# Optimization experiments

Measured on AMD Instinct MI355X. Metric: run time of the kernel, lower is better.

## Reference

```python
import jax, jax.numpy as jnp
import numpy as np

D_MODEL = 1024
N_HEADS = 16
D_K = D_MODEL // N_HEADS
THETA = 10000.0
BATCH, SEQ = 2, 2048


def setup_inputs() -> dict:
    key = jax.random.key(0)
    k1, k2, k3 = jax.random.split(key, 3)
    std_qkv = float(np.sqrt(2.0 / (3 * D_MODEL + D_MODEL)))
    std_o = float(np.sqrt(2.0 / (D_MODEL + D_MODEL)))
    return {
        "x": jax.random.normal(k1, (BATCH, SEQ, D_MODEL), dtype=jnp.float32),
        "w_qkv": jax.random.normal(k2, (3 * D_MODEL, D_MODEL), dtype=jnp.float32) * std_qkv,
        "w_o": jax.random.normal(k3, (D_MODEL, D_MODEL), dtype=jnp.float32) * std_o,
        "token_positions": jnp.arange(SEQ, dtype=jnp.int32),
    }


def _rope(x, token_positions):
    # x: [..., s, d_k]; interleaved rotary embedding
    d_k = x.shape[-1]
    freqs = jnp.arange(0, d_k, 2, dtype=jnp.float32) / d_k          # [d_k/2]
    inv_freqs = 1.0 / (THETA ** freqs)
    angles = token_positions.astype(jnp.float32)[:, None] * inv_freqs  # [s, d_k/2]
    cos, sin = jnp.cos(angles), jnp.sin(angles)
    x_even, x_odd = x[..., 0::2], x[..., 1::2]
    rot_even = x_even * cos - x_odd * sin
    rot_odd = x_even * sin + x_odd * cos
    # interleave back: out[..., 2i] = rot_even[i], out[..., 2i+1] = rot_odd[i]
    return jnp.stack([rot_even, rot_odd], axis=-1).reshape(x.shape)


def reference(x, w_qkv, w_o, token_positions):
    b, s, _ = x.shape
    qkv = jnp.einsum('oi,bsi->bso', w_qkv, x)                        # [b, s, 3*d_model]
    q, k, v = jnp.split(qkv, 3, axis=-1)
    def to_heads(t):
        return t.reshape(b, s, N_HEADS, D_K).transpose(0, 2, 1, 3)  # [b, h, s, d]
    q, k, v = to_heads(q), to_heads(k), to_heads(v)
    q = _rope(q, token_positions)
    k = _rope(k, token_positions)
    scores = jnp.einsum('bhqd,bhkd->bhqk', q, k) / jnp.sqrt(jnp.float32(D_K))
    causal = jnp.tril(jnp.ones((s, s), dtype=bool))
    scores = jnp.where(causal, scores, -jnp.inf)
    attn = jax.nn.softmax(scores, axis=-1)
    y = jnp.einsum('bhqk,bhkd->bhqd', attn, v)
    y = y.transpose(0, 2, 1, 3).reshape(b, s, D_MODEL)
    return jnp.einsum('oi,bsi->bso', w_o, y)
```

## Files before the change

kernel.cpp:

```cpp
#include <hip/hip_runtime.h>
#include <math.h>

#define DEV __device__ __forceinline__

typedef __attribute__((ext_vector_type(8))) short bf16x8;
typedef __attribute__((ext_vector_type(4))) float f32x4;
typedef __attribute__((ext_vector_type(4))) unsigned int u32x4;

typedef __attribute__((address_space(3))) unsigned int lds_u32;
typedef const __attribute__((address_space(1))) unsigned int glb_u32;

DEV void gload16(const unsigned short* g, unsigned short* l) {
  __builtin_amdgcn_global_load_lds((glb_u32*)g, (lds_u32*)l, 16, 0, 0);
}

DEV bf16x8 lds_read8(const unsigned short* base, unsigned int byteoff) {
  return *reinterpret_cast<const bf16x8*>(
      reinterpret_cast<const char*>(base) + byteoff);
}

DEV float fexp2(float x) { return __builtin_amdgcn_exp2f(x); }

DEV unsigned short f2bf(float f) {
  union { float f; unsigned int u; } v; v.f = f;
  unsigned int u = v.u;
  unsigned int r = (u + 0x7fffu + ((u >> 16) & 1u)) >> 16;
  return (unsigned short)r;
}
DEV float bf2f(unsigned short h) {
  union { unsigned int u; float f; } v; v.u = ((unsigned int)h) << 16;
  return v.f;
}
DEV unsigned int cvtpk_bf16(float lo, float hi) {
  unsigned int r;
  asm("v_cvt_pk_bf16_f32 %0, %1, %2" : "=v"(r) : "v"(lo), "v"(hi));
  return r;
}

__global__ void cvt3_f32_bf16(const float* __restrict__ ina,
                              unsigned short* __restrict__ outa, int n4a,
                              const float* __restrict__ inb,
                              unsigned short* __restrict__ outb, int n4b,
                              const float* __restrict__ inc,
                              unsigned short* __restrict__ outc, int n4c) {
  int stride = gridDim.x * blockDim.x;
  int total = n4a + n4b + n4c;
  for (int i = blockIdx.x * blockDim.x + threadIdx.x; i < total; i += stride) {
    const float* src;
    unsigned short* dst;
    int j = i;
    if (j < n4a) {
      src = ina; dst = outa;
    } else if ((j -= n4a) < n4b) {
      src = inb; dst = outb;
    } else {
      j -= n4b; src = inc; dst = outc;
    }
    float4 f = reinterpret_cast<const float4*>(src)[j];
    ushort4 o;
    o.x = f2bf(f.x); o.y = f2bf(f.y); o.z = f2bf(f.z); o.w = f2bf(f.w);
    reinterpret_cast<ushort4*>(dst)[j] = o;
  }
}

__global__ __launch_bounds__(512, 2) void gemm8_qkv(const unsigned short* __restrict__ A,
                                                    const unsigned short* __restrict__ B,
                                                    unsigned short* __restrict__ C) {
  constexpr int K = 1024;
  constexpr int NK = 16;
  __shared__ unsigned short Ls[2][32768];

  const int tid = threadIdx.x;
  const int lane = tid & 63, wid = tid >> 6;
  const int wm = (wid >> 2) * 128;
  const int wn = (wid & 3) * 64;
  const int fr = lane & 15, kq = lane >> 4;

  int bid = blockIdx.x;
  int swz = (bid & 7) * 24 + (bid >> 3);
  int tm = swz & 15, tn = swz >> 4;
  const int arow0 = tm * 256, brow0 = tn * 256;

  const int subrow = lane >> 3;
  const int scol = ((lane & 7) ^ subrow) * 8;
  const unsigned short* aSrc = A + (size_t)(arow0 + wid * 8 + subrow) * K + scol;
  const unsigned short* bSrc = B + (size_t)(brow0 + wid * 8 + subrow) * K + scol;

  unsigned aoff[2], boff[2];
#pragma unroll
  for (int ks = 0; ks < 2; ks++) {
    unsigned x = ((unsigned)((ks * 4 + kq) ^ (fr & 7))) * 16;
    aoff[ks] = (unsigned)((wm + fr) * 128) + x;
    boff[ks] = 32768u + (unsigned)((wn + fr) * 128) + x;
  }

  f32x4 acc[8][4] = {};

#define STAGE_A8(BUF, H, T)                                                  \
  {                                                                          \
    gload16(aSrc + (size_t)((H) * 128) * K + (T) * 64,                       \
            &Ls[BUF][((H) * 128 + wid * 8) * 64]);                           \
    gload16(aSrc + (size_t)((H) * 128 + 64) * K + (T) * 64,                  \
            &Ls[BUF][((H) * 128 + 64 + wid * 8) * 64]);                      \
  }
#define STAGE_B8(BUF, H, T)                                                  \
  {                                                                          \
    gload16(bSrc + (size_t)((H) * 128) * K + (T) * 64,                       \
            &Ls[BUF][16384 + ((H) * 128 + wid * 8) * 64]);                   \
    gload16(bSrc + (size_t)((H) * 128 + 64) * K + (T) * 64,                  \
            &Ls[BUF][16384 + ((H) * 128 + 64 + wid * 8) * 64]);              \
  }

  STAGE_A8(0, 0, 0) STAGE_A8(0, 1, 0)
  STAGE_B8(0, 0, 0) STAGE_B8(0, 1, 0)
  STAGE_B8(1, 0, 1) STAGE_B8(1, 1, 1)
  asm volatile("s_waitcnt vmcnt(4)" ::: "memory");
  __builtin_amdgcn_s_barrier();

#define PHASE8(BUF, P, DO_STAGE)                                              \
  {                                                                           \
    bf16x8 af[2][2];                                                          \
    _Pragma("unroll") for (int mm = 0; mm < 2; mm++)                          \
      _Pragma("unroll") for (int ks = 0; ks < 2; ks++)                        \
        af[mm][ks] = lds_read8(Ls[BUF], aoff[ks] + ((P) * 2 + mm) * 2048);    \
    DO_STAGE                                                                  \
    __builtin_amdgcn_s_setprio(1);                                            \
    _Pragma("unroll") for (int mm = 0; mm < 2; mm++)                          \
      _Pragma("unroll") for (int j = 0; j < 4; j++)                           \
        _Pragma("unroll") for (int ks = 0; ks < 2; ks++)                      \
          acc[(P) * 2 + mm][j] = __builtin_amdgcn_mfma_f32_16x16x32_bf16(     \
              af[mm][ks], bq[j][ks], acc[(P) * 2 + mm][j], 0, 0, 0);          \
    __builtin_amdgcn_s_setprio(0);                                            \
  }

#define TILE8(T, BUF)                                                          \
  {                                                                            \
    bf16x8 bq[4][2];                                                           \
    _Pragma("unroll") for (int j = 0; j < 4; j++)                              \
      _Pragma("unroll") for (int ks = 0; ks < 2; ks++)                         \
        bq[j][ks] = lds_read8(Ls[BUF], boff[ks] + j * 2048);                   \
    PHASE8(BUF, 0, {                                                           \
      if ((T) + 1 < NK) { STAGE_A8(BUF ^ 1, 0, (T) + 1) STAGE_A8(BUF ^ 1, 1, (T) + 1) } \
    })                                                                         \
    __builtin_amdgcn_s_barrier();                                              \
    PHASE8(BUF, 1, { if ((T) + 2 < NK) STAGE_B8(BUF, 0, (T) + 2) })            \
    __builtin_amdgcn_s_barrier();                                              \
    PHASE8(BUF, 2, { if ((T) + 2 < NK) STAGE_B8(BUF, 1, (T) + 2) })            \
    __builtin_amdgcn_s_barrier();                                              \
    PHASE8(BUF, 3, {})                                                         \
    if ((T) + 2 < NK) {                                                        \
      asm volatile("s_waitcnt vmcnt(4)" ::: "memory");                         \
    } else {                                                                   \
      asm volatile("s_waitcnt vmcnt(0)" ::: "memory");                         \
    }                                                                          \
    __builtin_amdgcn_s_barrier();                                              \
    __builtin_amdgcn_sched_barrier(0);                                         \
  }

#pragma unroll 1
  for (int t = 0; t < NK; t += 2) {
    TILE8(t, 0)
    TILE8(t + 1, 1)
  }
#undef TILE8
#undef PHASE8
#undef STAGE_A8
#undef STAGE_B8

#pragma unroll
  for (int m = 0; m < 8; m++) {
#pragma unroll
    for (int j = 0; j < 4; j++) {
      size_t row = (size_t)(arow0 + wm + m * 16 + kq * 4);
      size_t col = (size_t)(brow0 + wn + j * 16 + fr);
#pragma unroll
      for (int r = 0; r < 4; r++)
        C[(row + r) * 3072 + col] = f2bf(acc[m][j][r]);
    }
  }
}

__global__ __launch_bounds__(256) void gemm_wo(const unsigned short* __restrict__ A,
                                               const unsigned short* __restrict__ B,
                                               float* __restrict__ C, int K) {
  __shared__ unsigned short Ab[2][4096];
  __shared__ unsigned short Bb[2][2048];
  const int tid = threadIdx.x;
  const int lane = tid & 63, wid = tid >> 6;
  const int wm = (wid >> 1) * 64, wn = (wid & 1) * 32;
  const int fr = lane & 15, kq = lane >> 4;
  const int arow0 = blockIdx.x * 128;
  const int brow0 = blockIdx.y * 64;

  const int srow = tid >> 2;
  const int schunk = (tid & 3) ^ (srow & 3);
  const unsigned short* aptr = A + (size_t)(arow0 + srow) * K + schunk * 8;
  const unsigned short* bptr = B + (size_t)(brow0 + srow) * K + schunk * 8;

  unsigned int offa[4], offb[2];
#pragma unroll
  for (int i = 0; i < 4; i++)
    offa[i] = (unsigned)((wm + i * 16 + fr) * 64 + ((kq ^ (fr & 3)) * 16));
#pragma unroll
  for (int j = 0; j < 2; j++)
    offb[j] = (unsigned)((wn + j * 16 + fr) * 64 + ((kq ^ (fr & 3)) * 16));

  f32x4 acc[4][2] = {};

#define WSTAGE(BI)                                                 \
  {                                                                \
    gload16(aptr, &Ab[BI][wid * 512]);                             \
    gload16(aptr + (size_t)64 * K, &Ab[BI][2048 + wid * 512]);     \
    gload16(bptr, &Bb[BI][wid * 512]);                             \
    aptr += 32;                                                    \
    bptr += 32;                                                    \
  }

#define WCOMP(BI)                                                                      \
  {                                                                                    \
    bf16x8 af[4], bfr[2];                                                              \
    _Pragma("unroll") for (int i = 0; i < 4; i++) af[i] = lds_read8(Ab[BI], offa[i]);  \
    _Pragma("unroll") for (int j = 0; j < 2; j++) bfr[j] = lds_read8(Bb[BI], offb[j]); \
    _Pragma("unroll") for (int i = 0; i < 4; i++)                                      \
      _Pragma("unroll") for (int j = 0; j < 2; j++)                                    \
        acc[i][j] = __builtin_amdgcn_mfma_f32_16x16x32_bf16(af[i], bfr[j], acc[i][j], 0, 0, 0); \
  }

  const int nk = K >> 5;
  WSTAGE(0);
  for (int ks = 0; ks < nk; ks += 2) {
    asm volatile("s_waitcnt lgkmcnt(0)" ::: "memory");
    __builtin_amdgcn_s_barrier();
    WSTAGE(1);
    asm volatile("s_waitcnt vmcnt(3)" ::: "memory");
    WCOMP(0);
    asm volatile("s_waitcnt lgkmcnt(0)" ::: "memory");
    __builtin_amdgcn_s_barrier();
    if (ks + 2 < nk) {
      WSTAGE(0);
      asm volatile("s_waitcnt vmcnt(3)" ::: "memory");
    } else {
      asm volatile("s_waitcnt vmcnt(0)" ::: "memory");
    }
    WCOMP(1);
  }
#undef WSTAGE
#undef WCOMP

#pragma unroll
  for (int i = 0; i < 4; i++) {
#pragma unroll
    for (int j = 0; j < 2; j++) {
#pragma unroll
      for (int r = 0; r < 4; r++) {
        size_t row = (size_t)(arow0 + wm + i * 16 + kq * 4 + r);
        size_t col = (size_t)(brow0 + wn + j * 16 + fr);
        C[row * 1024 + col] = acc[i][j][r];
      }
    }
  }
}

__global__ __launch_bounds__(256) void rope_vtrans_kernel(unsigned short* __restrict__ qkv,
                                                          const int* __restrict__ pos,
                                                          unsigned short* __restrict__ vt) {
  int bid0 = blockIdx.x;
  int t = threadIdx.x;
  if (bid0 < 4096) {
    int m = bid0;
    int s = m & 2047;
    __shared__ float Cl[32], Sl[32];
    if (t < 32) {
      float position = (float)pos[s];
      float inv = __expf(-(float)t * (9.210340371976184f / 32.0f));
      float ang = position * inv;
      Cl[t] = cosf(ang);
      Sl[t] = sinf(ang);
    }
    __syncthreads();
    const float QS = 0.18033688011112042f;
    int h = t >> 4, g = t & 15;
    float c0 = Cl[2 * g], s0 = Sl[2 * g], c1 = Cl[2 * g + 1], s1 = Sl[2 * g + 1];
    size_t base = (size_t)m * 3072 + h * 64 + 4 * g;
    ushort4 qv = *reinterpret_cast<ushort4*>(&qkv[base]);
    float qe0 = bf2f(qv.x), qo0 = bf2f(qv.y), qe1 = bf2f(qv.z), qo1 = bf2f(qv.w);
    qv.x = f2bf((qe0 * c0 - qo0 * s0) * QS);
    qv.y = f2bf((qe0 * s0 + qo0 * c0) * QS);
    qv.z = f2bf((qe1 * c1 - qo1 * s1) * QS);
    qv.w = f2bf((qe1 * s1 + qo1 * c1) * QS);
    *reinterpret_cast<ushort4*>(&qkv[base]) = qv;
    size_t kb = base + 1024;
    ushort4 kv = *reinterpret_cast<ushort4*>(&qkv[kb]);
    float ke0 = bf2f(kv.x), ko0 = bf2f(kv.y), ke1 = bf2f(kv.z), ko1 = bf2f(kv.w);
    kv.x = f2bf(ke0 * c0 - ko0 * s0);
    kv.y = f2bf(ke0 * s0 + ko0 * c0);
    kv.z = f2bf(ke1 * c1 - ko1 * s1);
    kv.w = f2bf(ke1 * s1 + ko1 * c1);
    *reinterpret_cast<ushort4*>(&qkv[kb]) = kv;
  } else {
    int bid = bid0 - 4096;
    int sb = bid & 31;
    int bh = bid >> 5;
    int h = bh & 15, b = bh >> 4;
    __shared__ unsigned short tile[64][72];
    int sl = t >> 2, c0 = (t & 3) * 16;
    const unsigned short* src = qkv + (size_t)(b * 2048 + sb * 64) * 3072 + 2048 + h * 64;
    *reinterpret_cast<bf16x8*>(&tile[sl][c0]) =
        *reinterpret_cast<const bf16x8*>(&src[(size_t)sl * 3072 + c0]);
    *reinterpret_cast<bf16x8*>(&tile[sl][c0 + 8]) =
        *reinterpret_cast<const bf16x8*>(&src[(size_t)sl * 3072 + c0 + 8]);
    __syncthreads();
    int d = t >> 2, p0 = (t & 3) * 16;
    unsigned short* dst = vt + ((size_t)bh * 64 + d) * 2048 + sb * 64 + p0;
    bf16x8 o0, o1;
#pragma unroll
    for (int i = 0; i < 8; i++) {
      int p = p0 + i;
      int s_in = (p & 32) + ((p >> 2) & 1) * 16 + ((p >> 3) & 3) * 4 + (p & 3);
      o0[i] = (short)tile[s_in][d];
    }
#pragma unroll
    for (int i = 0; i < 8; i++) {
      int p = p0 + 8 + i;
      int s_in = (p & 32) + ((p >> 2) & 1) * 16 + ((p >> 3) & 3) * 4 + (p & 3);
      o1[i] = (short)tile[s_in][d];
    }
    *reinterpret_cast<bf16x8*>(dst) = o0;
    *reinterpret_cast<bf16x8*>(dst + 8) = o1;
  }
}

__global__ __launch_bounds__(256, 4) void attn_kernel(const unsigned short* __restrict__ qkv,
                                                      const unsigned short* __restrict__ vt,
                                                      unsigned short* __restrict__ Y,
                                                      unsigned short* __restrict__ Opart,
                                                      float* __restrict__ Lsum) {
  int bid = blockIdx.x;
  int bh = bid & 31;
  int pair = (bid >> 5) & 15;
  int halfsel = bid >> 9;
  int h = bh & 15, b = bh >> 4;
  int tid = threadIdx.x, lane = tid & 63, wid = tid >> 6;
  int fr = lane & 15, kq = lane >> 4;

  const size_t mrow0 = (size_t)b * 2048;
  const unsigned short* Kp = qkv + mrow0 * 3072 + 1024 + h * 64;
  const unsigned short* Vp = vt + ((size_t)bh * 64) * 2048;

  __shared__ unsigned short Klds[2][4096];
  __shared__ unsigned short Vlds[2][4096];

  const int srow = tid >> 3;
  const int schunk = (tid & 7) ^ (srow & 7);

  unsigned int offk[8], offv[8];
#pragma unroll
  for (int gg = 0; gg < 4; gg++)
#pragma unroll
    for (int ks = 0; ks < 2; ks++) {
      int R = gg * 16 + fr;
      offk[gg * 2 + ks] = (unsigned)(R * 128 + (((4 * ks + kq) ^ (R & 7)) * 16));
    }
#pragma unroll
  for (int db = 0; db < 4; db++)
#pragma unroll
    for (int hf = 0; hf < 2; hf++) {
      int d = db * 16 + fr;
      offv[db * 2 + hf] = (unsigned)(d * 128 + (((4 * hf + kq) ^ (d & 7)) * 16));
    }

  bf16x8 vones;
#pragma unroll
  for (int i = 0; i < 8; i++) vones[i] = (short)0x3F80;

#define STAGE(BI)                                                     \
  {                                                                   \
    gload16(kstage, &Klds[BI][wid * 512]);                            \
    gload16(kstage + (size_t)32 * 3072, &Klds[BI][2048 + wid * 512]); \
    gload16(vstage, &Vlds[BI][wid * 512]);                            \
    gload16(vstage + 32 * 2048, &Vlds[BI][2048 + wid * 512]);         \
    kstage += (size_t)64 * 3072;                                      \
    vstage += 64;                                                     \
  }

#define TILE_COMPUTE(T, BI)                                                           \
  {                                                                                   \
    const bool masked_ = ((T) == qt_);                                                \
    f32x4 sc[4] = {};                                                                 \
    __builtin_amdgcn_s_setprio(1);                                                    \
    _Pragma("unroll") for (int gg = 0; gg < 4; gg++) {                                \
      _Pragma("unroll") for (int ks = 0; ks < 2; ks++) {                              \
        bf16x8 kf = lds_read8(Klds[BI], offk[gg * 2 + ks]);                           \
        sc[gg] = __builtin_amdgcn_mfma_f32_16x16x32_bf16(kf, qf[ks], sc[gg], 0, 0, 0);\
      }                                                                               \
    }                                                                                 \
    __builtin_amdgcn_s_setprio(0);                                                    \
    float p[16];                                                                      \
    _Pragma("unroll") for (int gg = 0; gg < 4; gg++)                                  \
      _Pragma("unroll") for (int rr = 0; rr < 4; rr++) {                              \
        float v = sc[gg][rr];                                                         \
        if (masked_) {                                                                \
          int k = (T) * 64 + gg * 16 + kq * 4 + rr;                                   \
          if (k > q_lane_) v = -1e30f;                                                \
        }                                                                             \
        p[gg * 4 + rr] = fexp2(v);                                                    \
      }                                                                               \
    u32x4 W0 = {cvtpk_bf16(p[0], p[1]), cvtpk_bf16(p[2], p[3]),                       \
                cvtpk_bf16(p[4], p[5]), cvtpk_bf16(p[6], p[7])};                      \
    u32x4 W1 = {cvtpk_bf16(p[8], p[9]), cvtpk_bf16(p[10], p[11]),                     \
                cvtpk_bf16(p[12], p[13]), cvtpk_bf16(p[14], p[15])};                  \
    bf16x8 pa0 = *reinterpret_cast<bf16x8*>(&W0);                                     \
    bf16x8 pa1 = *reinterpret_cast<bf16x8*>(&W1);                                     \
    __builtin_amdgcn_s_setprio(1);                                                    \
    _Pragma("unroll") for (int db = 0; db < 4; db++) {                                \
      bf16x8 vf0 = lds_read8(Vlds[BI], offv[db * 2]);                                 \
      acc[db] = __builtin_amdgcn_mfma_f32_16x16x32_bf16(vf0, pa0, acc[db], 0, 0, 0);  \
      bf16x8 vf1 = lds_read8(Vlds[BI], offv[db * 2 + 1]);                             \
      acc[db] = __builtin_amdgcn_mfma_f32_16x16x32_bf16(vf1, pa1, acc[db], 0, 0, 0);  \
    }                                                                                 \
    lacc = __builtin_amdgcn_mfma_f32_16x16x32_bf16(vones, pa0, lacc, 0, 0, 0);        \
    lacc = __builtin_amdgcn_mfma_f32_16x16x32_bf16(vones, pa1, lacc, 0, 0, 0);        \
    __builtin_amdgcn_s_setprio(0);                                                    \
  }

#define ATTN_RANGE(QT_, TLO_, THI_, MODE_, HALF_)                                     \
  {                                                                                   \
    const int qt_ = (QT_);                                                            \
    const int qbase_ = qt_ * 64 + wid * 16;                                           \
    const int q_lane_ = qbase_ + fr;                                                  \
    const unsigned short* Qp = qkv + (mrow0 + qbase_) * 3072 + h * 64;                \
    bf16x8 qf[2];                                                                     \
    _Pragma("unroll") for (int ks = 0; ks < 2; ks++)                                  \
      qf[ks] = *reinterpret_cast<const bf16x8*>(                                      \
          &Qp[(size_t)fr * 3072 + ks * 32 + kq * 8]);                                 \
    const unsigned short* kstage =                                                    \
        Kp + (size_t)srow * 3072 + schunk * 8 + (size_t)(TLO_) * 64 * 3072;           \
    const unsigned short* vstage =                                                    \
        Vp + (size_t)srow * 2048 + schunk * 8 + (TLO_) * 64;                          \
    f32x4 acc[4] = {};                                                                \
    f32x4 lacc = {};                                                                  \
    const int nt_ = (THI_) - (TLO_);                                                  \
    STAGE(0);                                                                         \
    for (int u = 0; u < nt_; u += 2) {                                                \
      asm volatile("s_waitcnt lgkmcnt(0)" ::: "memory");                              \
      __builtin_amdgcn_s_barrier();                                                   \
      if (u + 1 < nt_) {                                                              \
        STAGE(1);                                                                     \
        asm volatile("s_waitcnt vmcnt(4)" ::: "memory");                              \
      } else {                                                                        \
        asm volatile("s_waitcnt vmcnt(0)" ::: "memory");                              \
      }                                                                               \
      TILE_COMPUTE((TLO_) + u, 0);                                                    \
      if (u + 1 >= nt_) break;                                                        \
      asm volatile("s_waitcnt lgkmcnt(0)" ::: "memory");                              \
      __builtin_amdgcn_s_barrier();                                                   \
      if (u + 2 < nt_) {                                                              \
        STAGE(0);                                                                     \
        asm volatile("s_waitcnt vmcnt(4)" ::: "memory");                              \
      } else {                                                                        \
        asm volatile("s_waitcnt vmcnt(0)" ::: "memory");                              \
      }                                                                               \
      TILE_COMPUTE((TLO_) + u + 1, 1);                                                \
    }                                                                                 \
    if (MODE_ == 0) {                                                                 \
      float inv = 1.0f / lacc[0];                                                     \
      unsigned short* yp = Y + (mrow0 + qbase_ + fr) * 1024 + h * 64 + kq * 4;        \
      _Pragma("unroll") for (int db = 0; db < 4; db++) {                              \
        ushort4 o;                                                                    \
        o.x = f2bf(acc[db][0] * inv);                                                 \
        o.y = f2bf(acc[db][1] * inv);                                                 \
        o.z = f2bf(acc[db][2] * inv);                                                 \
        o.w = f2bf(acc[db][3] * inv);                                                 \
        *reinterpret_cast<ushort4*>(yp + db * 16) = o;                                \
      }                                                                               \
    } else {                                                                          \
      const int slot = (pair * 2 + (HALF_)) * 32 + bh;                                \
      unsigned short* op = Opart + (size_t)slot * 4096;                               \
      _Pragma("unroll") for (int db = 0; db < 4; db++)                                \
        _Pragma("unroll") for (int rr = 0; rr < 4; rr++) {                            \
          int d = db * 16 + kq * 4 + rr;                                              \
          op[(wid * 16 + 0) * 0 + d * 64 + (qbase_ & 63) + fr - (qbase_ & 63)] =      \
              f2bf(acc[db][rr]);                                                      \
        }                                                                             \
      if (kq == 0) Lsum[slot * 256 + wid * 16 + 0 * 64 + (fr) + wid * 0] = lacc[0];   \
    }                                                                                 \
  }


  if (halfsel == 0) {
    const int Lt = 31 - pair;
    {
      const int qt_ = Lt;
      const int qbase_ = qt_ * 64 + wid * 16;
      const int q_lane_ = qbase_ + fr;
      const unsigned short* Qp = qkv + (mrow0 + qbase_) * 3072 + h * 64;
      bf16x8 qf[2];
#pragma unroll
      for (int ks = 0; ks < 2; ks++)
        qf[ks] = *reinterpret_cast<const bf16x8*>(&Qp[(size_t)fr * 3072 + ks * 32 + kq * 8]);
      const unsigned short* kstage = Kp + (size_t)srow * 3072 + schunk * 8;
      const unsigned short* vstage = Vp + (size_t)srow * 2048 + schunk * 8;
      f32x4 acc[4] = {};
      f32x4 lacc = {};
      const int nt_ = 16;
      STAGE(0);
      for (int u = 0; u < nt_; u += 2) {
        asm volatile("s_waitcnt lgkmcnt(0)" ::: "memory");
        __builtin_amdgcn_s_barrier();
        if (u + 1 < nt_) {
          STAGE(1);
          asm volatile("s_waitcnt vmcnt(4)" ::: "memory");
        } else {
          asm volatile("s_waitcnt vmcnt(0)" ::: "memory");
        }
        TILE_COMPUTE(u, 0);
        if (u + 1 >= nt_) break;
        asm volatile("s_waitcnt lgkmcnt(0)" ::: "memory");
        __builtin_amdgcn_s_barrier();
        if (u + 2 < nt_) {
          STAGE(0);
          asm volatile("s_waitcnt vmcnt(4)" ::: "memory");
        } else {
          asm volatile("s_waitcnt vmcnt(0)" ::: "memory");
        }
        TILE_COMPUTE(u + 1, 1);
      }
      const int slot = (pair * 2 + 0) * 32 + bh;
      unsigned short* op = Opart + (size_t)slot * 4096;
      int qcol = wid * 16 + fr;
#pragma unroll
      for (int db = 0; db < 4; db++)
#pragma unroll
        for (int rr = 0; rr < 4; rr++) {
          int d = db * 16 + kq * 4 + rr;
          op[d * 64 + qcol] = f2bf(acc[db][rr]);
        }
      if (kq == 0) Lsum[slot * 64 + qcol] = lacc[0];
    }
  } else {
    const int Lt = 31 - pair;
    {
      const int qt_ = Lt;
      const int qbase_ = qt_ * 64 + wid * 16;
      const int q_lane_ = qbase_ + fr;
      const unsigned short* Qp = qkv + (mrow0 + qbase_) * 3072 + h * 64;
      bf16x8 qf[2];
#pragma unroll
      for (int ks = 0; ks < 2; ks++)
        qf[ks] = *reinterpret_cast<const bf16x8*>(&Qp[(size_t)fr * 3072 + ks * 32 + kq * 8]);
      const unsigned short* kstage = Kp + (size_t)srow * 3072 + schunk * 8 + (size_t)16 * 64 * 3072;
      const unsigned short* vstage = Vp + (size_t)srow * 2048 + schunk * 8 + 16 * 64;
      f32x4 acc[4] = {};
      f32x4 lacc = {};
      const int nt_ = 16 - pair;
      STAGE(0);
      for (int u = 0; u < nt_; u += 2) {
        asm volatile("s_waitcnt lgkmcnt(0)" ::: "memory");
        __builtin_amdgcn_s_barrier();
        if (u + 1 < nt_) {
          STAGE(1);
          asm volatile("s_waitcnt vmcnt(4)" ::: "memory");
        } else {
          asm volatile("s_waitcnt vmcnt(0)" ::: "memory");
        }
        TILE_COMPUTE(16 + u, 0);
        if (u + 1 >= nt_) break;
        asm volatile("s_waitcnt lgkmcnt(0)" ::: "memory");
        __builtin_amdgcn_s_barrier();
        if (u + 2 < nt_) {
          STAGE(0);
          asm volatile("s_waitcnt vmcnt(4)" ::: "memory");
        } else {
          asm volatile("s_waitcnt vmcnt(0)" ::: "memory");
        }
        TILE_COMPUTE(16 + u + 1, 1);
      }
      const int slot = (pair * 2 + 1) * 32 + bh;
      unsigned short* op = Opart + (size_t)slot * 4096;
      int qcol = wid * 16 + fr;
#pragma unroll
      for (int db = 0; db < 4; db++)
#pragma unroll
        for (int rr = 0; rr < 4; rr++) {
          int d = db * 16 + kq * 4 + rr;
          op[d * 64 + qcol] = f2bf(acc[db][rr]);
        }
      if (kq == 0) Lsum[slot * 64 + qcol] = lacc[0];
    }
    asm volatile("s_waitcnt lgkmcnt(0) vmcnt(0)" ::: "memory");
    __builtin_amdgcn_s_barrier();
    {
      const int qt_ = pair;
      const int qbase_ = qt_ * 64 + wid * 16;
      const int q_lane_ = qbase_ + fr;
      const unsigned short* Qp = qkv + (mrow0 + qbase_) * 3072 + h * 64;
      bf16x8 qf[2];
#pragma unroll
      for (int ks = 0; ks < 2; ks++)
        qf[ks] = *reinterpret_cast<const bf16x8*>(&Qp[(size_t)fr * 3072 + ks * 32 + kq * 8]);
      const unsigned short* kstage = Kp + (size_t)srow * 3072 + schunk * 8;
      const unsigned short* vstage = Vp + (size_t)srow * 2048 + schunk * 8;
      f32x4 acc[4] = {};
      f32x4 lacc = {};
      const int nt_ = pair + 1;
      STAGE(0);
      for (int u = 0; u < nt_; u += 2) {
        asm volatile("s_waitcnt lgkmcnt(0)" ::: "memory");
        __builtin_amdgcn_s_barrier();
        if (u + 1 < nt_) {
          STAGE(1);
          asm volatile("s_waitcnt vmcnt(4)" ::: "memory");
        } else {
          asm volatile("s_waitcnt vmcnt(0)" ::: "memory");
        }
        TILE_COMPUTE(u, 0);
        if (u + 1 >= nt_) break;
        asm volatile("s_waitcnt lgkmcnt(0)" ::: "memory");
        __builtin_amdgcn_s_barrier();
        if (u + 2 < nt_) {
          STAGE(0);
          asm volatile("s_waitcnt vmcnt(4)" ::: "memory");
        } else {
          asm volatile("s_waitcnt vmcnt(0)" ::: "memory");
        }
        TILE_COMPUTE(u + 1, 1);
      }
      float inv = 1.0f / lacc[0];
      unsigned short* yp = Y + (mrow0 + qbase_ + fr) * 1024 + h * 64 + kq * 4;
#pragma unroll
      for (int db = 0; db < 4; db++) {
        ushort4 o;
        o.x = f2bf(acc[db][0] * inv);
        o.y = f2bf(acc[db][1] * inv);
        o.z = f2bf(acc[db][2] * inv);
        o.w = f2bf(acc[db][3] * inv);
        *reinterpret_cast<ushort4*>(yp + db * 16) = o;
      }
    }
  }
#undef ATTN_RANGE
#undef TILE_COMPUTE
#undef STAGE
}

__global__ __launch_bounds__(256) void attn_combine(const unsigned short* __restrict__ Opart,
                                                    const float* __restrict__ Lsum,
                                                    unsigned short* __restrict__ Y) {
  int bid = blockIdx.x;
  int pair = bid >> 5;
  int bh = bid & 31;
  int Lt = 31 - pair;
  int h = bh & 15, b = bh >> 4;
  int t = threadIdx.x;
  int q = t >> 2, d0 = (t & 3) * 16;
  size_t s0 = (size_t)((pair * 2 + 0) * 32 + bh);
  size_t s1 = (size_t)((pair * 2 + 1) * 32 + bh);
  float inv = 1.0f / (Lsum[s0 * 64 + q] + Lsum[s1 * 64 + q]);
  const unsigned short* p0 = Opart + s0 * 4096;
  const unsigned short* p1 = Opart + s1 * 4096;
  bf16x8 o0, o1;
#pragma unroll
  for (int i = 0; i < 8; i++) {
    int d = d0 + i;
    o0[i] = (short)f2bf((bf2f(p0[d * 64 + q]) + bf2f(p1[d * 64 + q])) * inv);
  }
#pragma unroll
  for (int i = 0; i < 8; i++) {
    int d = d0 + 8 + i;
    o1[i] = (short)f2bf((bf2f(p0[d * 64 + q]) + bf2f(p1[d * 64 + q])) * inv);
  }
  unsigned short* yp = Y + ((size_t)(b * 2048 + Lt * 64 + q)) * 1024 + h * 64 + d0;
  *reinterpret_cast<bf16x8*>(yp) = o0;
  *reinterpret_cast<bf16x8*>(yp + 8) = o1;
}

extern "C" void kernel_launch(void* const* d_in, const int* in_sizes, int n_in,
                              void* d_out, int out_size, void* d_ws, size_t ws_size,
                              hipStream_t stream) {
  const float* x     = (const float*)d_in[0];
  const float* w_qkv = (const float*)d_in[1];
  const float* w_o   = (const float*)d_in[2];
  const int*   pos   = (const int*)d_in[3];
  float* out = (float*)d_out;

  unsigned char* ws = (unsigned char*)d_ws;
  unsigned short* x_bf    = (unsigned short*)(ws);
  unsigned short* wqkv_bf = (unsigned short*)(ws + 8388608);
  unsigned short* wo_bf   = (unsigned short*)(ws + 14680064);
  unsigned short* qkv     = (unsigned short*)(ws + 16777216);
  unsigned short* vt      = (unsigned short*)(ws + 41943040);
  unsigned short* y       = (unsigned short*)(ws + 50331648);
  unsigned short* Opart = x_bf;
  float* Lsum = (float*)wqkv_bf;

  cvt3_f32_bf16<<<1536, 256, 0, stream>>>(x, x_bf, 4096 * 1024 / 4,
                                          w_qkv, wqkv_bf, 3072 * 1024 / 4,
                                          w_o, wo_bf, 1024 * 1024 / 4);

  gemm8_qkv<<<192, 512, 0, stream>>>(x_bf, wqkv_bf, qkv);

  rope_vtrans_kernel<<<5120, 256, 0, stream>>>(qkv, pos, vt);

  attn_kernel<<<1024, 256, 0, stream>>>(qkv, vt, y, Opart, Lsum);
  attn_combine<<<512, 256, 0, stream>>>(Opart, Lsum, y);

  gemm_wo<<<dim3(32, 16), 256, 0, stream>>>(y, wo_bf, out, 1024);
}
```

Baseline: 104.3 us.

## Fuse RoPE and query scaling into the QKV GEMM epilogue

Applies the rotary embedding and query scaling inside the QKV GEMM store epilogue. Each lane gets its even/odd partner value from the MFMA accumulator layout through a lane-xor shuffle. The cos/sin table is now built once in the conversion kernel and stored in the otherwise-unused vt buffer. The standalone RoPE pass is removed, which saves a full read-modify-write of Q and K in global memory and leaves a V-transpose-only kernel. The trade-off is extra table loads, shuffles and math in the GEMM epilogue; an unused macro is also removed.

```diff
diff --git a/kernel.cpp b/kernel.cpp
--- a/kernel.cpp
+++ b/kernel.cpp
@@ -42,30 +42,42 @@
                               const float* __restrict__ inb,
                               unsigned short* __restrict__ outb, int n4b,
                               const float* __restrict__ inc,
-                              unsigned short* __restrict__ outc, int n4c) {
+                              unsigned short* __restrict__ outc, int n4c,
+                              const int* __restrict__ pos,
+                              float2* __restrict__ tab) {
   int stride = gridDim.x * blockDim.x;
   int total = n4a + n4b + n4c;
-  for (int i = blockIdx.x * blockDim.x + threadIdx.x; i < total; i += stride) {
-    const float* src;
-    unsigned short* dst;
-    int j = i;
-    if (j < n4a) {
-      src = ina; dst = outa;
-    } else if ((j -= n4a) < n4b) {
-      src = inb; dst = outb;
+  int totalt = total + 2048 * 32;
+  for (int i = blockIdx.x * blockDim.x + threadIdx.x; i < totalt; i += stride) {
+    if (i < total) {
+      const float* src;
+      unsigned short* dst;
+      int j = i;
+      if (j < n4a) {
+        src = ina; dst = outa;
+      } else if ((j -= n4a) < n4b) {
+        src = inb; dst = outb;
+      } else {
+        j -= n4b; src = inc; dst = outc;
+      }
+      float4 f = reinterpret_cast<const float4*>(src)[j];
+      ushort4 o;
+      o.x = f2bf(f.x); o.y = f2bf(f.y); o.z = f2bf(f.z); o.w = f2bf(f.w);
+      reinterpret_cast<ushort4*>(dst)[j] = o;
     } else {
-      j -= n4b; src = inc; dst = outc;
-    }
-    float4 f = reinterpret_cast<const float4*>(src)[j];
-    ushort4 o;
-    o.x = f2bf(f.x); o.y = f2bf(f.y); o.z = f2bf(f.z); o.w = f2bf(f.w);
-    reinterpret_cast<ushort4*>(dst)[j] = o;
+      int j2 = i - total;
+      int s = j2 >> 5, p = j2 & 31;
+      float inv = __expf(-(float)p * (9.210340371976184f / 32.0f));
+      float ang = (float)pos[s] * inv;
+      tab[j2] = make_float2(cosf(ang), sinf(ang));
+    }
   }
 }
 
 __global__ __launch_bounds__(512, 2) void gemm8_qkv(const unsigned short* __restrict__ A,
                                                     const unsigned short* __restrict__ B,
-                                                    unsigned short* __restrict__ C) {
+                                                    unsigned short* __restrict__ C,
+                                                    const float2* __restrict__ tab) {
   constexpr int K = 1024;
   constexpr int NK = 16;
   __shared__ unsigned short Ls[2][32768];
@@ -167,15 +179,39 @@
 #undef STAGE_A8
 #undef STAGE_B8
 
-#pragma unroll
-  for (int m = 0; m < 8; m++) {
-#pragma unroll
-    for (int j = 0; j < 4; j++) {
-      size_t row = (size_t)(arow0 + wm + m * 16 + kq * 4);
-      size_t col = (size_t)(brow0 + wn + j * 16 + fr);
-#pragma unroll
-      for (int r = 0; r < 4; r++)
-        C[(row + r) * 3072 + col] = f2bf(acc[m][j][r]);
+  if (brow0 < 2048) {
+    const bool isq = (brow0 < 1024);
+#pragma unroll
+    for (int m = 0; m < 8; m++) {
+#pragma unroll
+      for (int j = 0; j < 4; j++) {
+        int p = (j * 16 + fr) >> 1;
+        size_t row0 = (size_t)(arow0 + wm + m * 16 + kq * 4);
+        size_t col = (size_t)(brow0 + wn + j * 16 + fr);
+#pragma unroll
+        for (int r = 0; r < 4; r++) {
+          int s_ = (int)((row0 + r) & 2047);
+          float2 cs = tab[s_ * 32 + p];
+          float v = acc[m][j][r];
+          float part = __shfl_xor(v, 1);
+          float outv = (fr & 1) ? (part * cs.y + v * cs.x)
+                                : (v * cs.x - part * cs.y);
+          if (isq) outv *= 0.18033688011112042f;
+          C[(row0 + r) * 3072 + col] = f2bf(outv);
+        }
+      }
+    }
+  } else {
+#pragma unroll
+    for (int m = 0; m < 8; m++) {
+#pragma unroll
+      for (int j = 0; j < 4; j++) {
+        size_t row = (size_t)(arow0 + wm + m * 16 + kq * 4);
+        size_t col = (size_t)(brow0 + wn + j * 16 + fr);
+#pragma unroll
+        for (int r = 0; r < 4; r++)
+          C[(row + r) * 3072 + col] = f2bf(acc[m][j][r]);
+      }
     }
   }
 }
@@ -261,73 +297,38 @@
   }
 }
 
-__global__ __launch_bounds__(256) void rope_vtrans_kernel(unsigned short* __restrict__ qkv,
-                                                          const int* __restrict__ pos,
-                                                          unsigned short* __restrict__ vt) {
-  int bid0 = blockIdx.x;
+__global__ __launch_bounds__(256) void vtrans_kernel(const unsigned short* __restrict__ qkv,
+                                                     unsigned short* __restrict__ vt) {
+  int bid = blockIdx.x;
+  int sb = bid & 31;
+  int bh = bid >> 5;
+  int h = bh & 15, b = bh >> 4;
+  __shared__ unsigned short tile[64][72];
   int t = threadIdx.x;
-  if (bid0 < 4096) {
-    int m = bid0;
-    int s = m & 2047;
-    __shared__ float Cl[32], Sl[32];
-    if (t < 32) {
-      float position = (float)pos[s];
-      float inv = __expf(-(float)t * (9.210340371976184f / 32.0f));
-      float ang = position * inv;
-      Cl[t] = cosf(ang);
-      Sl[t] = sinf(ang);
-    }
-    __syncthreads();
-    const float QS = 0.18033688011112042f;
-    int h = t >> 4, g = t & 15;
-    float c0 = Cl[2 * g], s0 = Sl[2 * g], c1 = Cl[2 * g + 1], s1 = Sl[2 * g + 1];
-    size_t base = (size_t)m * 3072 + h * 64 + 4 * g;
-    ushort4 qv = *reinterpret_cast<ushort4*>(&qkv[base]);
-    float qe0 = bf2f(qv.x), qo0 = bf2f(qv.y), qe1 = bf2f(qv.z), qo1 = bf2f(qv.w);
-    qv.x = f2bf((qe0 * c0 - qo0 * s0) * QS);
-    qv.y = f2bf((qe0 * s0 + qo0 * c0) * QS);
-    qv.z = f2bf((qe1 * c1 - qo1 * s1) * QS);
-    qv.w = f2bf((qe1 * s1 + qo1 * c1) * QS);
-    *reinterpret_cast<ushort4*>(&qkv[base]) = qv;
-    size_t kb = base + 1024;
-    ushort4 kv = *reinterpret_cast<ushort4*>(&qkv[kb]);
-    float ke0 = bf2f(kv.x), ko0 = bf2f(kv.y), ke1 = bf2f(kv.z), ko1 = bf2f(kv.w);
-    kv.x = f2bf(ke0 * c0 - ko0 * s0);
-    kv.y = f2bf(ke0 * s0 + ko0 * c0);
-    kv.z = f2bf(ke1 * c1 - ko1 * s1);
-    kv.w = f2bf(ke1 * s1 + ko1 * c1);
-    *reinterpret_cast<ushort4*>(&qkv[kb]) = kv;
-  } else {
-    int bid = bid0 - 4096;
-    int sb = bid & 31;
-    int bh = bid >> 5;
-    int h = bh & 15, b = bh >> 4;
-    __shared__ unsigned short tile[64][72];
-    int sl = t >> 2, c0 = (t & 3) * 16;
-    const unsigned short* src = qkv + (size_t)(b * 2048 + sb * 64) * 3072 + 2048 + h * 64;
-    *reinterpret_cast<bf16x8*>(&tile[sl][c0]) =
-        *reinterpret_cast<const bf16x8*>(&src[(size_t)sl * 3072 + c0]);
-    *reinterpret_cast<bf16x8*>(&tile[sl][c0 + 8]) =
-        *reinterpret_cast<const bf16x8*>(&src[(size_t)sl * 3072 + c0 + 8]);
-    __syncthreads();
-    int d = t >> 2, p0 = (t & 3) * 16;
-    unsigned short* dst = vt + ((size_t)bh * 64 + d) * 2048 + sb * 64 + p0;
-    bf16x8 o0, o1;
-#pragma unroll
-    for (int i = 0; i < 8; i++) {
-      int p = p0 + i;
-      int s_in = (p & 32) + ((p >> 2) & 1) * 16 + ((p >> 3) & 3) * 4 + (p & 3);
-      o0[i] = (short)tile[s_in][d];
-    }
-#pragma unroll
-    for (int i = 0; i < 8; i++) {
-      int p = p0 + 8 + i;
-      int s_in = (p & 32) + ((p >> 2) & 1) * 16 + ((p >> 3) & 3) * 4 + (p & 3);
-      o1[i] = (short)tile[s_in][d];
-    }
-    *reinterpret_cast<bf16x8*>(dst) = o0;
-    *reinterpret_cast<bf16x8*>(dst + 8) = o1;
-  }
+  int sl = t >> 2, c0 = (t & 3) * 16;
+  const unsigned short* src = qkv + (size_t)(b * 2048 + sb * 64) * 3072 + 2048 + h * 64;
+  *reinterpret_cast<bf16x8*>(&tile[sl][c0]) =
+      *reinterpret_cast<const bf16x8*>(&src[(size_t)sl * 3072 + c0]);
+  *reinterpret_cast<bf16x8*>(&tile[sl][c0 + 8]) =
+      *reinterpret_cast<const bf16x8*>(&src[(size_t)sl * 3072 + c0 + 8]);
+  __syncthreads();
+  int d = t >> 2, p0 = (t & 3) * 16;
+  unsigned short* dst = vt + ((size_t)bh * 64 + d) * 2048 + sb * 64 + p0;
+  bf16x8 o0, o1;
+#pragma unroll
+  for (int i = 0; i < 8; i++) {
+    int p = p0 + i;
+    int s_in = (p & 32) + ((p >> 2) & 1) * 16 + ((p >> 3) & 3) * 4 + (p & 3);
+    o0[i] = (short)tile[s_in][d];
+  }
+#pragma unroll
+  for (int i = 0; i < 8; i++) {
+    int p = p0 + 8 + i;
+    int s_in = (p & 32) + ((p >> 2) & 1) * 16 + ((p >> 3) & 3) * 4 + (p & 3);
+    o1[i] = (short)tile[s_in][d];
+  }
+  *reinterpret_cast<bf16x8*>(dst) = o0;
+  *reinterpret_cast<bf16x8*>(dst + 8) = o1;
 }
 
 __global__ __launch_bounds__(256, 4) void attn_kernel(const unsigned short* __restrict__ qkv,
@@ -423,70 +424,6 @@
     __builtin_amdgcn_s_setprio(0);                                                    \
   }
 
-#define ATTN_RANGE(QT_, TLO_, THI_, MODE_, HALF_)                                     \
-  {                                                                                   \
-    const int qt_ = (QT_);                                                            \
-    const int qbase_ = qt_ * 64 + wid * 16;                                           \
-    const int q_lane_ = qbase_ + fr;                                                  \
-    const unsigned short* Qp = qkv + (mrow0 + qbase_) * 3072 + h * 64;                \
-    bf16x8 qf[2];                                                                     \
-    _Pragma("unroll") for (int ks = 0; ks < 2; ks++)                                  \
-      qf[ks] = *reinterpret_cast<const bf16x8*>(                                      \
-          &Qp[(size_t)fr * 3072 + ks * 32 + kq * 8]);                                 \
-    const unsigned short* kstage =                                                    \
-        Kp + (size_t)srow * 3072 + schunk * 8 + (size_t)(TLO_) * 64 * 3072;           \
-    const unsigned short* vstage =                                                    \
-        Vp + (size_t)srow * 2048 + schunk * 8 + (TLO_) * 64;                          \
-    f32x4 acc[4] = {};                                                                \
-    f32x4 lacc = {};                                                                  \
-    const int nt_ = (THI_) - (TLO_);                                                  \
-    STAGE(0);                                                                         \
-    for (int u = 0; u < nt_; u += 2) {                                                \
-      asm volatile("s_waitcnt lgkmcnt(0)" ::: "memory");                              \
-      __builtin_amdgcn_s_barrier();                                                   \
-      if (u + 1 < nt_) {                                                              \
-        STAGE(1);                                                                     \
-        asm volatile("s_waitcnt vmcnt(4)" ::: "memory");                              \
-      } else {                                                                        \
-        asm volatile("s_waitcnt vmcnt(0)" ::: "memory");                              \
-      }                                                                               \
-      TILE_COMPUTE((TLO_) + u, 0);                                                    \
-      if (u + 1 >= nt_) break;                                                        \
-      asm volatile("s_waitcnt lgkmcnt(0)" ::: "memory");                              \
-      __builtin_amdgcn_s_barrier();                                                   \
-      if (u + 2 < nt_) {                                                              \
-        STAGE(0);                                                                     \
-        asm volatile("s_waitcnt vmcnt(4)" ::: "memory");                              \
-      } else {                                                                        \
-        asm volatile("s_waitcnt vmcnt(0)" ::: "memory");                              \
-      }                                                                               \
-      TILE_COMPUTE((TLO_) + u + 1, 1);                                                \
-    }                                                                                 \
-    if (MODE_ == 0) {                                                                 \
-      float inv = 1.0f / lacc[0];                                                     \
-      unsigned short* yp = Y + (mrow0 + qbase_ + fr) * 1024 + h * 64 + kq * 4;        \
-      _Pragma("unroll") for (int db = 0; db < 4; db++) {                              \
-        ushort4 o;                                                                    \
-        o.x = f2bf(acc[db][0] * inv);                                                 \
-        o.y = f2bf(acc[db][1] * inv);                                                 \
-        o.z = f2bf(acc[db][2] * inv);                                                 \
-        o.w = f2bf(acc[db][3] * inv);                                                 \
-        *reinterpret_cast<ushort4*>(yp + db * 16) = o;                                \
-      }                                                                               \
-    } else {                                                                          \
-      const int slot = (pair * 2 + (HALF_)) * 32 + bh;                                \
-      unsigned short* op = Opart + (size_t)slot * 4096;                               \
-      _Pragma("unroll") for (int db = 0; db < 4; db++)                                \
-        _Pragma("unroll") for (int rr = 0; rr < 4; rr++) {                            \
-          int d = db * 16 + kq * 4 + rr;                                              \
-          op[(wid * 16 + 0) * 0 + d * 64 + (qbase_ & 63) + fr - (qbase_ & 63)] =      \
-              f2bf(acc[db][rr]);                                                      \
-        }                                                                             \
-      if (kq == 0) Lsum[slot * 256 + wid * 16 + 0 * 64 + (fr) + wid * 0] = lacc[0];   \
-    }                                                                                 \
-  }
-
-
   if (halfsel == 0) {
     const int Lt = 31 - pair;
     {
@@ -638,7 +575,6 @@
       }
     }
   }
-#undef ATTN_RANGE
 #undef TILE_COMPUTE
 #undef STAGE
 }
@@ -692,14 +628,16 @@
   unsigned short* y       = (unsigned short*)(ws + 50331648);
   unsigned short* Opart = x_bf;
   float* Lsum = (float*)wqkv_bf;
+  float2* tab = (float2*)vt;
 
   cvt3_f32_bf16<<<1536, 256, 0, stream>>>(x, x_bf, 4096 * 1024 / 4,
                                           w_qkv, wqkv_bf, 3072 * 1024 / 4,
-                                          w_o, wo_bf, 1024 * 1024 / 4);
-
-  gemm8_qkv<<<192, 512, 0, stream>>>(x_bf, wqkv_bf, qkv);
-
-  rope_vtrans_kernel<<<5120, 256, 0, stream>>>(qkv, pos, vt);
+                                          w_o, wo_bf, 1024 * 1024 / 4,
+                                          pos, tab);
+
+  gemm8_qkv<<<192, 512, 0, stream>>>(x_bf, wqkv_bf, qkv, tab);
+
+  vtrans_kernel<<<1024, 256, 0, stream>>>(qkv, vt);
 
   attn_kernel<<<1024, 256, 0, stream>>>(qkv, vt, y, Opart, Lsum);
   attn_combine<<<512, 256, 0, stream>>>(Opart, Lsum, y);
```

Result: no change. 105.7 us (+1.3%).
